# Kernel optimization log

Hardware: AMD Instinct MI355X
Metric: run time of the kernel (lower is better)

## Reference

```python
import jax, jax.numpy as jnp
import numpy as np

VOCAB = 32000
EMBED = 256
HIDDEN = 512
BATCH = 64
T_CAP = 32


def setup_inputs() -> dict:
    key = jax.random.key(0)
    ks = jax.random.split(key, 10)
    s_e = 1.0 / np.sqrt(HIDDEN)  # torch LSTM/Linear init scale
    inp = {
        "features": jax.random.normal(ks[0], (BATCH, EMBED), jnp.float32),
        "captions": jax.random.randint(ks[1], (BATCH, T_CAP), 0, VOCAB, jnp.int32),
        "lengths": jax.random.randint(ks[2], (BATCH,), 1, 33, jnp.int32),
        "embedding": jax.random.normal(ks[3], (VOCAB, EMBED), jnp.float32),
        "W_ih": jax.random.uniform(ks[4], (4 * HIDDEN, EMBED), jnp.float32, -s_e, s_e),
        "W_hh": jax.random.uniform(ks[5], (4 * HIDDEN, HIDDEN), jnp.float32, -s_e, s_e),
        "b_ih": jax.random.uniform(ks[6], (4 * HIDDEN,), jnp.float32, -s_e, s_e),
        "b_hh": jax.random.uniform(ks[7], (4 * HIDDEN,), jnp.float32, -s_e, s_e),
        "W_out": jax.random.uniform(ks[8], (VOCAB, HIDDEN), jnp.float32, -s_e, s_e),
        "b_out": jax.random.uniform(ks[9], (VOCAB,), jnp.float32, -s_e, s_e),
    }
    return inp


def _lstm_over_seq(x, W_ih, W_hh, b_ih, b_hh):
    # x: [B, S, E] -> hiddens [B, S, H]; torch gate order i, f, g, o
    B = x.shape[0]
    H = W_hh.shape[1]
    # precompute input projections for all timesteps in one GEMM
    x_proj = jnp.einsum("bse,ge->bsg", x, W_ih) + b_ih + b_hh  # [B, S, 4H]

    def step(carry, xp_t):
        h, c = carry
        gates = xp_t + h @ W_hh.T  # [B, 4H]
        i, f, g, o = jnp.split(gates, 4, axis=-1)
        c = jax.nn.sigmoid(f) * c + jax.nn.sigmoid(i) * jnp.tanh(g)
        h = jax.nn.sigmoid(o) * jnp.tanh(c)
        return (h, c), h

    h0 = jnp.zeros((B, H), x.dtype)
    (_, _), hs = jax.lax.scan(step, (h0, h0), jnp.swapaxes(x_proj, 0, 1))
    return jnp.swapaxes(hs, 0, 1)  # [B, S, H]


def reference(features, captions, lengths, embedding, W_ih, W_hh, b_ih, b_hh, W_out, b_out):
    emb = embedding[captions]  # [B, T, E] embedding lookup
    x = jnp.concatenate([features[:, None, :], emb], axis=1)  # [B, T+1, E]
    hs = _lstm_over_seq(x, W_ih, W_hh, b_ih, b_hh)  # [B, T+1, H]
    logits = jnp.einsum("bsh,vh->bsv", hs, W_out) + b_out  # [B, T+1, V]
    return logits
```

## Files before the change

### kernel.cpp

```cpp
#include <hip/hip_runtime.h>
#include <hip/hip_bf16.h>
#include <math.h>

#define VOCAB  32000
#define EMBED  256
#define HIDDEN 512
#define BATCH  64
#define TCAP   32
#define SEQ    33
#define G4     2048
#define MROWS  2112

typedef unsigned short ushort_t;

__device__ __forceinline__ float bf2f(ushort_t u) {
    union { unsigned int i; float f; } v;
    v.i = ((unsigned int)u) << 16;
    return v.f;
}

__device__ __forceinline__ void bfpair(unsigned int u, float& lo, float& hi) {
    union { unsigned int i; float f; } a, b;
    a.i = u << 16;
    b.i = u & 0xffff0000u;
    lo = a.f; hi = b.f;
}

template<bool BF>
__device__ __forceinline__ void ldw8(const void* p, size_t idx, float* w) {
    if constexpr (BF) {
        uint4 u = *(const uint4*)((const ushort_t*)p + idx);
        bfpair(u.x, w[0], w[1]); bfpair(u.y, w[2], w[3]);
        bfpair(u.z, w[4], w[5]); bfpair(u.w, w[6], w[7]);
    } else {
        float4 a = *(const float4*)((const float*)p + idx);
        float4 b = *(const float4*)((const float*)p + idx + 4);
        w[0]=a.x; w[1]=a.y; w[2]=a.z; w[3]=a.w;
        w[4]=b.x; w[5]=b.y; w[6]=b.z; w[7]=b.w;
    }
}

template<bool BF>
__device__ __forceinline__ float ldw1(const void* p, size_t i) {
    if constexpr (BF) return bf2f(((const ushort_t*)p)[i]);
    else return ((const float*)p)[i];
}

__device__ __forceinline__ float dot8f(const float* w, const float* h) {
    return w[0]*h[0]+w[1]*h[1]+w[2]*h[2]+w[3]*h[3]
         + w[4]*h[4]+w[5]*h[5]+w[6]*h[6]+w[7]*h[7];
}

__device__ __forceinline__ float sigm(float x) { return 1.0f / (1.0f + expf(-x)); }

__global__ void k_detect(const unsigned int* __restrict__ w, int* __restrict__ mode) {
    __shared__ int cnt[256];
    int c = 0;
    for (int i = threadIdx.x; i < 8192; i += 256) {
        unsigned int lo = w[i] & 0xffffu;
        int e = (lo >> 7) & 0xff;
        if (e >= 113 && e <= 131) c++;
    }
    cnt[threadIdx.x] = c;
    __syncthreads();
    for (int s = 128; s > 0; s >>= 1) {
        if (threadIdx.x < s) cnt[threadIdx.x] += cnt[threadIdx.x + s];
        __syncthreads();
    }
    if (threadIdx.x == 0) *mode = (cnt[0] > 6000) ? 1 : 0;
}

template<bool BF>
__global__ void k_xproj(const int* __restrict__ mode,
                        const void* __restrict__ features,
                        const int*  __restrict__ captions,
                        const void* __restrict__ embedding,
                        const void* __restrict__ W_ih,
                        const void* __restrict__ b_ih,
                        const void* __restrict__ b_hh,
                        float* __restrict__ xp) {
    if (*mode != (int)BF) return;
    __shared__ float xs[EMBED];
    int bt  = blockIdx.y;
    int b   = bt / SEQ;
    int t   = bt % SEQ;
    int tid = threadIdx.x;

    size_t src_off;
    const void* src;
    if (t == 0) { src = features;  src_off = (size_t)b * EMBED; }
    else        { src = embedding; src_off = (size_t)captions[b * TCAP + (t - 1)] * EMBED; }
    xs[tid] = ldw1<BF>(src, src_off + tid);
    __syncthreads();

    int g = blockIdx.x * 256 + tid;
    float acc = ldw1<BF>(b_ih, g) + ldw1<BF>(b_hh, g);
    size_t wbase = (size_t)g * EMBED;
    for (int e = 0; e < EMBED; e += 8) {
        float w[8];
        ldw8<BF>(W_ih, wbase + e, w);
        acc += dot8f(w, xs + e);
    }
    xp[(size_t)bt * G4 + g] = acc;
}

__global__ void k_wtr(const int* __restrict__ mode,
                      const void* __restrict__ Whh,
                      void* __restrict__ WT) {
    const bool bf = (*mode != 0);
    for (int r = 0; r < 4; r++) {
        size_t e = (size_t)blockIdx.x * 1024 + r * 256 + threadIdx.x;
        int g = (int)(e >> 9);
        int k = (int)(e & 511);
        if (bf) {
            ushort_t w = ((const ushort_t*)Whh)[e];
            ((ushort_t*)WT)[((size_t)(k >> 3) << 14) + ((size_t)g << 3) + (k & 7)] = w;
        } else {
            float w = ((const float*)Whh)[e];
            ((float*)WT)[((size_t)(k >> 2) << 13) + ((size_t)g << 2) + (k & 3)] = w;
        }
    }
}

__global__ __launch_bounds__(256)
void k_step3(const int* __restrict__ mode,
             const float* __restrict__ xp,
             const void* __restrict__ WT,
             float* __restrict__ c_buf,
             float* __restrict__ hs,
             int t) {
    const bool bf = (*mode != 0);
    __shared__ float hsh[4][HIDDEN];
    __shared__ float psum[4][32][4];
    int tid = threadIdx.x;
    int jl = tid & 31;
    int bb = (tid >> 5) & 3;
    int kh = tid >> 7;
    int j  = blockIdx.x * 32 + jl;
    int b  = blockIdx.y * 4 + bb;

    if (t > 0) {
        for (int r = 0; r < 2; r++) {
            int i4 = tid + r * 256;
            int sb = i4 >> 7, k4 = (i4 & 127) << 2;
            *(float4*)(&hsh[sb][k4]) =
                *(const float4*)(hs + ((size_t)(blockIdx.y * 4 + sb) * SEQ + (t - 1)) * HIDDEN + k4);
        }
        __syncthreads();
    }

    float ai = 0.f, af = 0.f, ag = 0.f, ao = 0.f;

    if (t > 0) {
        const float* hp = hsh[bb];
        if (bf) {
            const ushort_t* wt = (const ushort_t*)WT;
            const ushort_t* p0 = wt + (size_t)j * 8;
            const ushort_t* p1 = wt + (size_t)(HIDDEN + j) * 8;
            const ushort_t* p2 = wt + (size_t)(2 * HIDDEN + j) * 8;
            const ushort_t* p3 = wt + (size_t)(3 * HIDDEN + j) * 8;
#pragma unroll 2
            for (int k8 = kh * 32; k8 < kh * 32 + 32; ++k8) {
                size_t pb = (size_t)k8 * 16384;
                uint4 u0 = *(const uint4*)(p0 + pb);
                uint4 u1 = *(const uint4*)(p1 + pb);
                uint4 u2 = *(const uint4*)(p2 + pb);
                uint4 u3 = *(const uint4*)(p3 + pb);
                float4 h0 = *(const float4*)(hp + k8 * 8);
                float4 h1 = *(const float4*)(hp + k8 * 8 + 4);
                float w[8];
                bfpair(u0.x, w[0], w[1]); bfpair(u0.y, w[2], w[3]);
                bfpair(u0.z, w[4], w[5]); bfpair(u0.w, w[6], w[7]);
                ai += w[0]*h0.x + w[1]*h0.y + w[2]*h0.z + w[3]*h0.w
                    + w[4]*h1.x + w[5]*h1.y + w[6]*h1.z + w[7]*h1.w;
                bfpair(u1.x, w[0], w[1]); bfpair(u1.y, w[2], w[3]);
                bfpair(u1.z, w[4], w[5]); bfpair(u1.w, w[6], w[7]);
                af += w[0]*h0.x + w[1]*h0.y + w[2]*h0.z + w[3]*h0.w
                    + w[4]*h1.x + w[5]*h1.y + w[6]*h1.z + w[7]*h1.w;
                bfpair(u2.x, w[0], w[1]); bfpair(u2.y, w[2], w[3]);
                bfpair(u2.z, w[4], w[5]); bfpair(u2.w, w[6], w[7]);
                ag += w[0]*h0.x + w[1]*h0.y + w[2]*h0.z + w[3]*h0.w
                    + w[4]*h1.x + w[5]*h1.y + w[6]*h1.z + w[7]*h1.w;
                bfpair(u3.x, w[0], w[1]); bfpair(u3.y, w[2], w[3]);
                bfpair(u3.z, w[4], w[5]); bfpair(u3.w, w[6], w[7]);
                ao += w[0]*h0.x + w[1]*h0.y + w[2]*h0.z + w[3]*h0.w
                    + w[4]*h1.x + w[5]*h1.y + w[6]*h1.z + w[7]*h1.w;
            }
        } else {
            const float* wt = (const float*)WT;
            const float* p0 = wt + (size_t)j * 4;
            const float* p1 = wt + (size_t)(HIDDEN + j) * 4;
            const float* p2 = wt + (size_t)(2 * HIDDEN + j) * 4;
            const float* p3 = wt + (size_t)(3 * HIDDEN + j) * 4;
#pragma unroll 4
            for (int k4 = kh * 64; k4 < kh * 64 + 64; ++k4) {
                size_t pb = (size_t)k4 * 8192;
                float4 wi = *(const float4*)(p0 + pb);
                float4 wf = *(const float4*)(p1 + pb);
                float4 wg = *(const float4*)(p2 + pb);
                float4 wo = *(const float4*)(p3 + pb);
                float4 hv = *(const float4*)(hp + k4 * 4);
                ai += wi.x*hv.x + wi.y*hv.y + wi.z*hv.z + wi.w*hv.w;
                af += wf.x*hv.x + wf.y*hv.y + wf.z*hv.z + wf.w*hv.w;
                ag += wg.x*hv.x + wg.y*hv.y + wg.z*hv.z + wg.w*hv.w;
                ao += wo.x*hv.x + wo.y*hv.y + wo.z*hv.z + wo.w*hv.w;
            }
        }
        if (kh == 1) {
            psum[bb][jl][0] = ai; psum[bb][jl][1] = af;
            psum[bb][jl][2] = ag; psum[bb][jl][3] = ao;
        }
        __syncthreads();
        if (kh == 0) {
            ai += psum[bb][jl][0]; af += psum[bb][jl][1];
            ag += psum[bb][jl][2]; ao += psum[bb][jl][3];
        }
    }

    if (kh == 1) return;

    size_t xbase = ((size_t)b * SEQ + t) * G4;
    ai += xp[xbase + j];
    af += xp[xbase + HIDDEN + j];
    ag += xp[xbase + 2 * HIDDEN + j];
    ao += xp[xbase + 3 * HIDDEN + j];

    float c_prev = (t > 0) ? c_buf[b * HIDDEN + j] : 0.0f;
    float c = sigm(af) * c_prev + sigm(ai) * tanhf(ag);
    float h = sigm(ao) * tanhf(c);
    c_buf[b * HIDDEN + j] = c;
    hs[((size_t)b * SEQ + t) * HIDDEN + j] = h;
}

template<bool BF>
__global__ void k_step(const int* __restrict__ mode,
                       const float* __restrict__ xp,
                       const void* __restrict__ W_hh,
                       float* __restrict__ c_buf,
                       float* __restrict__ hs,
                       int t) {
    if (*mode != (int)BF) return;
    __shared__ float hsh[4][HIDDEN];
    int tid = threadIdx.x;
    int jl  = tid & 63, bb = tid >> 6;
    int j   = blockIdx.x * 64 + jl;
    int b   = blockIdx.y * 4 + bb;

    if (t > 0) {
        for (int r = 0; r < 2; r++) {
            int i4 = tid + r * 256;
            int sb = i4 >> 7, k4 = (i4 & 127) << 2;
            *(float4*)(&hsh[sb][k4]) =
                *(const float4*)(hs + ((size_t)(blockIdx.y * 4 + sb) * SEQ + (t - 1)) * HIDDEN + k4);
        }
        __syncthreads();
    }

    size_t xbase = ((size_t)b * SEQ + t) * G4;
    float ai = xp[xbase + j];
    float af = xp[xbase + HIDDEN + j];
    float ag = xp[xbase + 2 * HIDDEN + j];
    float ao = xp[xbase + 3 * HIDDEN + j];

    if (t > 0) {
        const float* hp = hsh[bb];
        size_t r0 = (size_t)j * HIDDEN;
        size_t r1 = (size_t)(HIDDEN + j) * HIDDEN;
        size_t r2 = (size_t)(2 * HIDDEN + j) * HIDDEN;
        size_t r3 = (size_t)(3 * HIDDEN + j) * HIDDEN;
        for (int k = 0; k < HIDDEN; k += 8) {
            float w[8];
            ldw8<BF>(W_hh, r0 + k, w); ai += dot8f(w, hp + k);
            ldw8<BF>(W_hh, r1 + k, w); af += dot8f(w, hp + k);
            ldw8<BF>(W_hh, r2 + k, w); ag += dot8f(w, hp + k);
            ldw8<BF>(W_hh, r3 + k, w); ao += dot8f(w, hp + k);
        }
    }

    float c_prev = (t > 0) ? c_buf[b * HIDDEN + j] : 0.0f;
    float c = sigm(af) * c_prev + sigm(ai) * tanhf(ag);
    float h = sigm(ao) * tanhf(c);
    c_buf[b * HIDDEN + j] = c;
    hs[((size_t)b * SEQ + t) * HIDDEN + j] = h;
}

#define BM 128
#define BN 128
#define KC 32
#define NBN 250
#define NBM 17
#define LOGITS_GRID (8 * 32 * NBM)

__device__ __forceinline__ int swz(int r) {
    return ((r >> 2) & 1) * 64 + (r >> 3) * 4 + (r & 3);
}

template<bool BF>
__global__ __launch_bounds__(256, 4)
void k_logits(const int* __restrict__ mode,
              const float* __restrict__ hs,
              const void* __restrict__ W_out,
              const void* __restrict__ b_out,
              void* __restrict__ out) {
    if (*mode != (int)BF) return;

    int bid = blockIdx.x;
    int xcd = bid & 7;
    int j8  = bid >> 3;
    int mb  = j8 % NBM;
    int nb  = xcd + 8 * (j8 / NBM);
    if (nb >= NBN) return;

    __shared__ float As[KC][BM];
    __shared__ float Bs[KC][BN];

    int t  = threadIdx.x;
    int tm = t >> 4;
    int tn = t & 15;
    int m_base = mb * BM;
    int n_base = nb * BN;

    float acc[8][8];
#pragma unroll
    for (int i = 0; i < 8; ++i)
#pragma unroll
        for (int q = 0; q < 8; ++q) acc[i][q] = 0.0f;

    for (int kt = 0; kt < HIDDEN / KC; ++kt) {
        __syncthreads();

#pragma unroll
        for (int i = 0; i < 4; ++i) {
            int flat = t + i * 256;
            int m  = flat >> 3;
            int kq = flat & 7;
            int gm = m_base + m;
            float4 v = make_float4(0.f, 0.f, 0.f, 0.f);
            if (gm < MROWS)
                v = *(const float4*)(hs + (size_t)gm * HIDDEN + kt * KC + kq * 4);
            int col = swz(m) ^ (kq << 2);
            As[kq*4+0][col] = v.x; As[kq*4+1][col] = v.y;
            As[kq*4+2][col] = v.z; As[kq*4+3][col] = v.w;
        }

        if constexpr (BF) {
#pragma unroll
            for (int i = 0; i < 2; ++i) {
                int flat = t + i * 256;
                int n  = flat >> 2;
                int ko = (flat & 3) * 8;
                const ushort_t* src = (const ushort_t*)W_out
                    + (size_t)(n_base + n) * HIDDEN + kt * KC + ko;
                uint4 u = *(const uint4*)src;
                float w[8];
                bfpair(u.x, w[0], w[1]); bfpair(u.y, w[2], w[3]);
                bfpair(u.z, w[4], w[5]); bfpair(u.w, w[6], w[7]);
                int sb = swz(n);
#pragma unroll
                for (int d = 0; d < 8; ++d) {
                    int kq = (ko + d) >> 2;
                    Bs[ko + d][sb ^ (kq << 2)] = w[d];
                }
            }
        } else {
#pragma unroll
            for (int i = 0; i < 4; ++i) {
                int flat = t + i * 256;
                int n  = flat >> 3;
                int kq = flat & 7;
                const float* src = (const float*)W_out
                    + (size_t)(n_base + n) * HIDDEN + kt * KC + kq * 4;
                float4 v = *(const float4*)src;
                int col = swz(n) ^ (kq << 2);
                Bs[kq*4+0][col] = v.x; Bs[kq*4+1][col] = v.y;
                Bs[kq*4+2][col] = v.z; Bs[kq*4+3][col] = v.w;
            }
        }
        __syncthreads();

#pragma unroll 8
        for (int k = 0; k < KC; ++k) {
            int kx = k & 28;
            float4 a0 = *(const float4*)&As[k][(tm * 4) ^ kx];
            float4 a1 = *(const float4*)&As[k][64 + ((tm * 4) ^ kx)];
            float4 b0 = *(const float4*)&Bs[k][(tn * 4) ^ kx];
            float4 b1 = *(const float4*)&Bs[k][64 + ((tn * 4) ^ kx)];
            float a[8] = {a0.x, a0.y, a0.z, a0.w, a1.x, a1.y, a1.z, a1.w};
            float b[8] = {b0.x, b0.y, b0.z, b0.w, b1.x, b1.y, b1.z, b1.w};
#pragma unroll
            for (int i = 0; i < 8; ++i)
#pragma unroll
                for (int q = 0; q < 8; ++q)
                    acc[i][q] = fmaf(a[i], b[q], acc[i][q]);
        }
    }

    float bias[8];
#pragma unroll
    for (int q = 0; q < 8; ++q) bias[q] = ldw1<BF>(b_out, n_base + tn * 8 + q);

#pragma unroll
    for (int i = 0; i < 8; ++i) {
        int gm = m_base + tm * 8 + i;
        if (gm >= MROWS) continue;
        size_t o = (size_t)gm * VOCAB + n_base + tn * 8;
        if constexpr (BF) {
            unsigned int p[4];
#pragma unroll
            for (int q = 0; q < 4; ++q) {
                __hip_bfloat16 lo = __float2bfloat16(acc[i][2*q]   + bias[2*q]);
                __hip_bfloat16 hi = __float2bfloat16(acc[i][2*q+1] + bias[2*q+1]);
                unsigned short ul = *(unsigned short*)&lo;
                unsigned short uh = *(unsigned short*)&hi;
                p[q] = (unsigned int)ul | ((unsigned int)uh << 16);
            }
            *(uint4*)((__hip_bfloat16*)out + o) = make_uint4(p[0], p[1], p[2], p[3]);
        } else {
            float* op = (float*)out + o;
            *(float4*)(op + 0) = make_float4(acc[i][0]+bias[0], acc[i][1]+bias[1],
                                             acc[i][2]+bias[2], acc[i][3]+bias[3]);
            *(float4*)(op + 4) = make_float4(acc[i][4]+bias[4], acc[i][5]+bias[5],
                                             acc[i][6]+bias[6], acc[i][7]+bias[7]);
        }
    }
}

extern "C" void kernel_launch(void* const* d_in, const int* in_sizes, int n_in,
                              void* d_out, int out_size, void* d_ws, size_t ws_size,
                              hipStream_t stream) {
    const void* features  = d_in[0];
    const int*  captions  = (const int*)d_in[1];
    const void* embedding = d_in[3];
    const void* W_ih      = d_in[4];
    const void* W_hh      = d_in[5];
    const void* b_ih      = d_in[6];
    const void* b_hh      = d_in[7];
    const void* W_out     = d_in[8];
    const void* b_out     = d_in[9];

    char* ws = (char*)d_ws;
    const size_t XP_OFF = 0;
    const size_t HS_OFF = (size_t)2112 * G4 * 4;
    const size_t CB_OFF = HS_OFF + (size_t)2112 * HIDDEN * 4;
    const size_t MODE_OFF = CB_OFF + (size_t)BATCH * HIDDEN * 4;
    const size_t WT_OFF = MODE_OFF + 16;
    const size_t NEED = WT_OFF + (size_t)4 * 1024 * 1024;

    float* xp    = (float*)(ws + XP_OFF);
    float* hs    = (float*)(ws + HS_OFF);
    float* c_buf = (float*)(ws + CB_OFF);
    int*   mode  = (int*)(ws + MODE_OFF);
    void*  WT    = (void*)(ws + WT_OFF);

    const bool fast = (ws_size >= NEED);

    k_detect<<<1, 256, 0, stream>>>((const unsigned int*)features, mode);

    if (fast)
        k_wtr<<<1024, 256, 0, stream>>>(mode, W_hh, WT);

    k_xproj<false><<<dim3(8, BATCH * SEQ), 256, 0, stream>>>(
        mode, features, captions, embedding, W_ih, b_ih, b_hh, xp);
    k_xproj<true><<<dim3(8, BATCH * SEQ), 256, 0, stream>>>(
        mode, features, captions, embedding, W_ih, b_ih, b_hh, xp);

    for (int t = 0; t < SEQ; t++) {
        if (fast) {
            k_step3<<<dim3(16, BATCH / 4), 256, 0, stream>>>(mode, xp, WT, c_buf, hs, t);
        } else {
            k_step<false><<<dim3(8, BATCH / 4), 256, 0, stream>>>(mode, xp, W_hh, c_buf, hs, t);
            k_step<true><<<dim3(8, BATCH / 4), 256, 0, stream>>>(mode, xp, W_hh, c_buf, hs, t);
        }
    }

    k_logits<false><<<dim3(LOGITS_GRID), 256, 0, stream>>>(mode, hs, W_out, b_out, d_out);
    k_logits<true><<<dim3(LOGITS_GRID), 256, 0, stream>>>(mode, hs, W_out, b_out, d_out);
}
```

Before: 1.996 ms.

## Fuse LSTM timesteps into one persistent kernel with a software grid barrier

Replaces the 33 per-timestep k_step3 launches with a single persistent k_lstm kernel of 256 blocks. The blocks synchronise between timesteps through an atomic counter and generation barrier, and the cell state stays in a register instead of a global buffer. The two templated xproj launches are also merged into one kernel that branches on the runtime mode. This removes launch overhead and c_buf traffic, but it relies on all 256 blocks being co-resident and adds spin-barrier latency on each step.

```diff
diff --git a/kernel.cpp b/kernel.cpp
--- a/kernel.cpp
+++ b/kernel.cpp
@@ -10,6 +10,7 @@
 #define SEQ    33
 #define G4     2048
 #define MROWS  2112
+#define NBLK_LSTM 256
 
 typedef unsigned short ushort_t;
 
@@ -53,7 +54,26 @@
 
 __device__ __forceinline__ float sigm(float x) { return 1.0f / (1.0f + expf(-x)); }
 
-__global__ void k_detect(const unsigned int* __restrict__ w, int* __restrict__ mode) {
+__device__ __forceinline__ void gridbar(unsigned* cnt, unsigned* gen) {
+    __syncthreads();
+    if (threadIdx.x == 0) {
+        __builtin_amdgcn_fence(__ATOMIC_SEQ_CST, "agent");
+        unsigned g = __hip_atomic_load(gen, __ATOMIC_RELAXED, __HIP_MEMORY_SCOPE_AGENT);
+        unsigned old = __hip_atomic_fetch_add(cnt, 1u, __ATOMIC_ACQ_REL, __HIP_MEMORY_SCOPE_AGENT);
+        if (old == NBLK_LSTM - 1u) {
+            __hip_atomic_store(cnt, 0u, __ATOMIC_RELAXED, __HIP_MEMORY_SCOPE_AGENT);
+            __hip_atomic_fetch_add(gen, 1u, __ATOMIC_ACQ_REL, __HIP_MEMORY_SCOPE_AGENT);
+        } else {
+            while (__hip_atomic_load(gen, __ATOMIC_ACQUIRE, __HIP_MEMORY_SCOPE_AGENT) == g)
+                __builtin_amdgcn_s_sleep(8);
+        }
+        __builtin_amdgcn_fence(__ATOMIC_SEQ_CST, "agent");
+    }
+    __syncthreads();
+}
+
+__global__ void k_detect(const unsigned int* __restrict__ w, int* __restrict__ mode,
+                         unsigned* __restrict__ bar) {
     __shared__ int cnt[256];
     int c = 0;
     for (int i = threadIdx.x; i < 8192; i += 256) {
@@ -67,19 +87,22 @@
         if (threadIdx.x < s) cnt[threadIdx.x] += cnt[threadIdx.x + s];
         __syncthreads();
     }
-    if (threadIdx.x == 0) *mode = (cnt[0] > 6000) ? 1 : 0;
-}
-
-template<bool BF>
-__global__ void k_xproj(const int* __restrict__ mode,
-                        const void* __restrict__ features,
-                        const int*  __restrict__ captions,
-                        const void* __restrict__ embedding,
-                        const void* __restrict__ W_ih,
-                        const void* __restrict__ b_ih,
-                        const void* __restrict__ b_hh,
-                        float* __restrict__ xp) {
-    if (*mode != (int)BF) return;
+    if (threadIdx.x == 0) {
+        *mode = (cnt[0] > 6000) ? 1 : 0;
+        __hip_atomic_store(bar + 0, 0u, __ATOMIC_RELAXED, __HIP_MEMORY_SCOPE_AGENT);
+        __hip_atomic_store(bar + 1, 0u, __ATOMIC_RELAXED, __HIP_MEMORY_SCOPE_AGENT);
+    }
+}
+
+__global__ void k_xproj2(const int* __restrict__ mode,
+                         const void* __restrict__ features,
+                         const int*  __restrict__ captions,
+                         const void* __restrict__ embedding,
+                         const void* __restrict__ W_ih,
+                         const void* __restrict__ b_ih,
+                         const void* __restrict__ b_hh,
+                         float* __restrict__ xp) {
+    const bool bf = (*mode != 0);
     __shared__ float xs[EMBED];
     int bt  = blockIdx.y;
     int b   = bt / SEQ;
@@ -90,16 +113,27 @@
     const void* src;
     if (t == 0) { src = features;  src_off = (size_t)b * EMBED; }
     else        { src = embedding; src_off = (size_t)captions[b * TCAP + (t - 1)] * EMBED; }
-    xs[tid] = ldw1<BF>(src, src_off + tid);
+    xs[tid] = bf ? bf2f(((const ushort_t*)src)[src_off + tid])
+                 : ((const float*)src)[src_off + tid];
     __syncthreads();
 
     int g = blockIdx.x * 256 + tid;
-    float acc = ldw1<BF>(b_ih, g) + ldw1<BF>(b_hh, g);
+    float acc;
     size_t wbase = (size_t)g * EMBED;
-    for (int e = 0; e < EMBED; e += 8) {
-        float w[8];
-        ldw8<BF>(W_ih, wbase + e, w);
-        acc += dot8f(w, xs + e);
+    if (bf) {
+        acc = bf2f(((const ushort_t*)b_ih)[g]) + bf2f(((const ushort_t*)b_hh)[g]);
+        for (int e = 0; e < EMBED; e += 8) {
+            float w[8];
+            ldw8<true>(W_ih, wbase + e, w);
+            acc += dot8f(w, xs + e);
+        }
+    } else {
+        acc = ((const float*)b_ih)[g] + ((const float*)b_hh)[g];
+        for (int e = 0; e < EMBED; e += 8) {
+            float w[8];
+            ldw8<false>(W_ih, wbase + e, w);
+            acc += dot8f(w, xs + e);
+        }
     }
     xp[(size_t)bt * G4 + g] = acc;
 }
@@ -123,12 +157,11 @@
 }
 
 __global__ __launch_bounds__(256)
-void k_step3(const int* __restrict__ mode,
-             const float* __restrict__ xp,
-             const void* __restrict__ WT,
-             float* __restrict__ c_buf,
-             float* __restrict__ hs,
-             int t) {
+void k_lstm(const int* __restrict__ mode,
+            const float* __restrict__ xp,
+            const void* __restrict__ WT,
+            float* __restrict__ hs,
+            unsigned* __restrict__ bar) {
     const bool bf = (*mode != 0);
     __shared__ float hsh[4][HIDDEN];
     __shared__ float psum[4][32][4];
@@ -136,100 +169,105 @@
     int jl = tid & 31;
     int bb = (tid >> 5) & 3;
     int kh = tid >> 7;
-    int j  = blockIdx.x * 32 + jl;
-    int b  = blockIdx.y * 4 + bb;
-
-    if (t > 0) {
-        for (int r = 0; r < 2; r++) {
-            int i4 = tid + r * 256;
-            int sb = i4 >> 7, k4 = (i4 & 127) << 2;
-            *(float4*)(&hsh[sb][k4]) =
-                *(const float4*)(hs + ((size_t)(blockIdx.y * 4 + sb) * SEQ + (t - 1)) * HIDDEN + k4);
-        }
-        __syncthreads();
-    }
-
-    float ai = 0.f, af = 0.f, ag = 0.f, ao = 0.f;
-
-    if (t > 0) {
-        const float* hp = hsh[bb];
-        if (bf) {
-            const ushort_t* wt = (const ushort_t*)WT;
-            const ushort_t* p0 = wt + (size_t)j * 8;
-            const ushort_t* p1 = wt + (size_t)(HIDDEN + j) * 8;
-            const ushort_t* p2 = wt + (size_t)(2 * HIDDEN + j) * 8;
-            const ushort_t* p3 = wt + (size_t)(3 * HIDDEN + j) * 8;
+    int blk = blockIdx.x;
+    int bx = blk & 15, by = blk >> 4;
+    int j  = bx * 32 + jl;
+    int b  = by * 4 + bb;
+    float c_reg = 0.0f;
+
+    for (int t = 0; t < SEQ; ++t) {
+        if (t > 0) {
+            gridbar(bar + 0, bar + 1);
+            for (int r = 0; r < 2; r++) {
+                int i4 = tid + r * 256;
+                int sb = i4 >> 7, k4 = (i4 & 127) << 2;
+                *(float4*)(&hsh[sb][k4]) =
+                    *(const float4*)(hs + ((size_t)(by * 4 + sb) * SEQ + (t - 1)) * HIDDEN + k4);
+            }
+            __syncthreads();
+        }
+
+        float ai = 0.f, af = 0.f, ag = 0.f, ao = 0.f;
+
+        if (t > 0) {
+            const float* hp = hsh[bb];
+            if (bf) {
+                const ushort_t* wt = (const ushort_t*)WT;
+                const ushort_t* p0 = wt + (size_t)j * 8;
+                const ushort_t* p1 = wt + (size_t)(HIDDEN + j) * 8;
+                const ushort_t* p2 = wt + (size_t)(2 * HIDDEN + j) * 8;
+                const ushort_t* p3 = wt + (size_t)(3 * HIDDEN + j) * 8;
 #pragma unroll 2
-            for (int k8 = kh * 32; k8 < kh * 32 + 32; ++k8) {
-                size_t pb = (size_t)k8 * 16384;
-                uint4 u0 = *(const uint4*)(p0 + pb);
-                uint4 u1 = *(const uint4*)(p1 + pb);
-                uint4 u2 = *(const uint4*)(p2 + pb);
-                uint4 u3 = *(const uint4*)(p3 + pb);
-                float4 h0 = *(const float4*)(hp + k8 * 8);
-                float4 h1 = *(const float4*)(hp + k8 * 8 + 4);
-                float w[8];
-                bfpair(u0.x, w[0], w[1]); bfpair(u0.y, w[2], w[3]);
-                bfpair(u0.z, w[4], w[5]); bfpair(u0.w, w[6], w[7]);
-                ai += w[0]*h0.x + w[1]*h0.y + w[2]*h0.z + w[3]*h0.w
-                    + w[4]*h1.x + w[5]*h1.y + w[6]*h1.z + w[7]*h1.w;
-                bfpair(u1.x, w[0], w[1]); bfpair(u1.y, w[2], w[3]);
-                bfpair(u1.z, w[4], w[5]); bfpair(u1.w, w[6], w[7]);
-                af += w[0]*h0.x + w[1]*h0.y + w[2]*h0.z + w[3]*h0.w
-                    + w[4]*h1.x + w[5]*h1.y + w[6]*h1.z + w[7]*h1.w;
-                bfpair(u2.x, w[0], w[1]); bfpair(u2.y, w[2], w[3]);
-                bfpair(u2.z, w[4], w[5]); bfpair(u2.w, w[6], w[7]);
-                ag += w[0]*h0.x + w[1]*h0.y + w[2]*h0.z + w[3]*h0.w
-                    + w[4]*h1.x + w[5]*h1.y + w[6]*h1.z + w[7]*h1.w;
-                bfpair(u3.x, w[0], w[1]); bfpair(u3.y, w[2], w[3]);
-                bfpair(u3.z, w[4], w[5]); bfpair(u3.w, w[6], w[7]);
-                ao += w[0]*h0.x + w[1]*h0.y + w[2]*h0.z + w[3]*h0.w
-                    + w[4]*h1.x + w[5]*h1.y + w[6]*h1.z + w[7]*h1.w;
-            }
-        } else {
-            const float* wt = (const float*)WT;
-            const float* p0 = wt + (size_t)j * 4;
-            const float* p1 = wt + (size_t)(HIDDEN + j) * 4;
-            const float* p2 = wt + (size_t)(2 * HIDDEN + j) * 4;
-            const float* p3 = wt + (size_t)(3 * HIDDEN + j) * 4;
+                for (int k8 = kh * 32; k8 < kh * 32 + 32; ++k8) {
+                    size_t pb = (size_t)k8 * 16384;
+                    uint4 u0 = *(const uint4*)(p0 + pb);
+                    uint4 u1 = *(const uint4*)(p1 + pb);
+                    uint4 u2 = *(const uint4*)(p2 + pb);
+                    uint4 u3 = *(const uint4*)(p3 + pb);
+                    float4 h0 = *(const float4*)(hp + k8 * 8);
+                    float4 h1 = *(const float4*)(hp + k8 * 8 + 4);
+                    float w[8];
+                    bfpair(u0.x, w[0], w[1]); bfpair(u0.y, w[2], w[3]);
+                    bfpair(u0.z, w[4], w[5]); bfpair(u0.w, w[6], w[7]);
+                    ai += w[0]*h0.x + w[1]*h0.y + w[2]*h0.z + w[3]*h0.w
+                        + w[4]*h1.x + w[5]*h1.y + w[6]*h1.z + w[7]*h1.w;
+                    bfpair(u1.x, w[0], w[1]); bfpair(u1.y, w[2], w[3]);
+                    bfpair(u1.z, w[4], w[5]); bfpair(u1.w, w[6], w[7]);
+                    af += w[0]*h0.x + w[1]*h0.y + w[2]*h0.z + w[3]*h0.w
+                        + w[4]*h1.x + w[5]*h1.y + w[6]*h1.z + w[7]*h1.w;
+                    bfpair(u2.x, w[0], w[1]); bfpair(u2.y, w[2], w[3]);
+                    bfpair(u2.z, w[4], w[5]); bfpair(u2.w, w[6], w[7]);
+                    ag += w[0]*h0.x + w[1]*h0.y + w[2]*h0.z + w[3]*h0.w
+                        + w[4]*h1.x + w[5]*h1.y + w[6]*h1.z + w[7]*h1.w;
+                    bfpair(u3.x, w[0], w[1]); bfpair(u3.y, w[2], w[3]);
+                    bfpair(u3.z, w[4], w[5]); bfpair(u3.w, w[6], w[7]);
+                    ao += w[0]*h0.x + w[1]*h0.y + w[2]*h0.z + w[3]*h0.w
+                        + w[4]*h1.x + w[5]*h1.y + w[6]*h1.z + w[7]*h1.w;
+                }
+            } else {
+                const float* wt = (const float*)WT;
+                const float* p0 = wt + (size_t)j * 4;
+                const float* p1 = wt + (size_t)(HIDDEN + j) * 4;
+                const float* p2 = wt + (size_t)(2 * HIDDEN + j) * 4;
+                const float* p3 = wt + (size_t)(3 * HIDDEN + j) * 4;
 #pragma unroll 4
-            for (int k4 = kh * 64; k4 < kh * 64 + 64; ++k4) {
-                size_t pb = (size_t)k4 * 8192;
-                float4 wi = *(const float4*)(p0 + pb);
-                float4 wf = *(const float4*)(p1 + pb);
-                float4 wg = *(const float4*)(p2 + pb);
-                float4 wo = *(const float4*)(p3 + pb);
-                float4 hv = *(const float4*)(hp + k4 * 4);
-                ai += wi.x*hv.x + wi.y*hv.y + wi.z*hv.z + wi.w*hv.w;
-                af += wf.x*hv.x + wf.y*hv.y + wf.z*hv.z + wf.w*hv.w;
-                ag += wg.x*hv.x + wg.y*hv.y + wg.z*hv.z + wg.w*hv.w;
-                ao += wo.x*hv.x + wo.y*hv.y + wo.z*hv.z + wo.w*hv.w;
-            }
-        }
-        if (kh == 1) {
-            psum[bb][jl][0] = ai; psum[bb][jl][1] = af;
-            psum[bb][jl][2] = ag; psum[bb][jl][3] = ao;
-        }
-        __syncthreads();
+                for (int k4 = kh * 64; k4 < kh * 64 + 64; ++k4) {
+                    size_t pb = (size_t)k4 * 8192;
+                    float4 wi = *(const float4*)(p0 + pb);
+                    float4 wf = *(const float4*)(p1 + pb);
+                    float4 wg = *(const float4*)(p2 + pb);
+                    float4 wo = *(const float4*)(p3 + pb);
+                    float4 hv = *(const float4*)(hp + k4 * 4);
+                    ai += wi.x*hv.x + wi.y*hv.y + wi.z*hv.z + wi.w*hv.w;
+                    af += wf.x*hv.x + wf.y*hv.y + wf.z*hv.z + wf.w*hv.w;
+                    ag += wg.x*hv.x + wg.y*hv.y + wg.z*hv.z + wg.w*hv.w;
+                    ao += wo.x*hv.x + wo.y*hv.y + wo.z*hv.z + wo.w*hv.w;
+                }
+            }
+            if (kh == 1) {
+                psum[bb][jl][0] = ai; psum[bb][jl][1] = af;
+                psum[bb][jl][2] = ag; psum[bb][jl][3] = ao;
+            }
+            __syncthreads();
+            if (kh == 0) {
+                ai += psum[bb][jl][0]; af += psum[bb][jl][1];
+                ag += psum[bb][jl][2]; ao += psum[bb][jl][3];
+            }
+        }
+
         if (kh == 0) {
-            ai += psum[bb][jl][0]; af += psum[bb][jl][1];
-            ag += psum[bb][jl][2]; ao += psum[bb][jl][3];
-        }
-    }
-
-    if (kh == 1) return;
-
-    size_t xbase = ((size_t)b * SEQ + t) * G4;
-    ai += xp[xbase + j];
-    af += xp[xbase + HIDDEN + j];
-    ag += xp[xbase + 2 * HIDDEN + j];
-    ao += xp[xbase + 3 * HIDDEN + j];
-
-    float c_prev = (t > 0) ? c_buf[b * HIDDEN + j] : 0.0f;
-    float c = sigm(af) * c_prev + sigm(ai) * tanhf(ag);
-    float h = sigm(ao) * tanhf(c);
-    c_buf[b * HIDDEN + j] = c;
-    hs[((size_t)b * SEQ + t) * HIDDEN + j] = h;
+            size_t xbase = ((size_t)b * SEQ + t) * G4;
+            ai += xp[xbase + j];
+            af += xp[xbase + HIDDEN + j];
+            ag += xp[xbase + 2 * HIDDEN + j];
+            ao += xp[xbase + 3 * HIDDEN + j];
+
+            float c = sigm(af) * c_reg + sigm(ai) * tanhf(ag);
+            float h = sigm(ao) * tanhf(c);
+            c_reg = c;
+            hs[((size_t)b * SEQ + t) * HIDDEN + j] = h;
+        }
+    }
 }
 
 template<bool BF>
@@ -450,24 +488,23 @@
     float* hs    = (float*)(ws + HS_OFF);
     float* c_buf = (float*)(ws + CB_OFF);
     int*   mode  = (int*)(ws + MODE_OFF);
+    unsigned* bar = (unsigned*)(ws + MODE_OFF + 8);
     void*  WT    = (void*)(ws + WT_OFF);
 
     const bool fast = (ws_size >= NEED);
 
-    k_detect<<<1, 256, 0, stream>>>((const unsigned int*)features, mode);
+    k_detect<<<1, 256, 0, stream>>>((const unsigned int*)features, mode, bar);
 
     if (fast)
         k_wtr<<<1024, 256, 0, stream>>>(mode, W_hh, WT);
 
-    k_xproj<false><<<dim3(8, BATCH * SEQ), 256, 0, stream>>>(
+    k_xproj2<<<dim3(8, BATCH * SEQ), 256, 0, stream>>>(
         mode, features, captions, embedding, W_ih, b_ih, b_hh, xp);
-    k_xproj<true><<<dim3(8, BATCH * SEQ), 256, 0, stream>>>(
-        mode, features, captions, embedding, W_ih, b_ih, b_hh, xp);
-
-    for (int t = 0; t < SEQ; t++) {
-        if (fast) {
-            k_step3<<<dim3(16, BATCH / 4), 256, 0, stream>>>(mode, xp, WT, c_buf, hs, t);
-        } else {
+
+    if (fast) {
+        k_lstm<<<NBLK_LSTM, 256, 0, stream>>>(mode, xp, WT, hs, bar);
+    } else {
+        for (int t = 0; t < SEQ; t++) {
             k_step<false><<<dim3(8, BATCH / 4), 256, 0, stream>>>(mode, xp, W_hh, c_buf, hs, t);
             k_step<true><<<dim3(8, BATCH / 4), 256, 0, stream>>>(mode, xp, W_hh, c_buf, hs, t);
         }
```

Result: slower. 3.001 ms (+50.4%).
